# Kernel optimization log

Measured on AMD Instinct MI355X. Metric: run time of the kernel, lower is better.

Reference implementation:

```python
import jax, jax.numpy as jnp
import numpy as np

COST_CLASS, COST_MASK, COST_DICE = 1.0, 1.0, 1.0
ALPHA, GAMMA = 0.25, 2.0


def setup_inputs() -> dict:
    key = jax.random.key(0)
    k1, k2, k3, k4 = jax.random.split(key, 4)
    B, Q, C, H, W, T, Hm, Wm = 2, 100, 134, 256, 256, 20, 512, 512
    return {
        "masks_queries_logits": jax.random.normal(k1, (B, Q, H, W), jnp.float32),
        "class_queries_logits": jax.random.normal(k2, (B, Q, C), jnp.float32),
        "mask_labels": jax.random.uniform(k3, (B, T, Hm, Wm), dtype=jnp.float32),
        "class_labels": jax.random.randint(k4, (B, T), 0, C),
    }


def _nearest_resize(x, H, W):
    # torch F.interpolate(mode='nearest'): src_idx = floor(dst_idx * in / out)
    Hi, Wi = x.shape[-2], x.shape[-1]
    ri = (jnp.arange(H) * Hi) // H
    ci = (jnp.arange(W) * Wi) // W
    return x[..., ri, :][..., ci]


def _cost_matrices(masks_queries_logits, class_queries_logits, mask_labels, class_labels):
    B, Q, H, W = masks_queries_logits.shape
    HW = H * W
    tgt = _nearest_resize(mask_labels, H, W)                       # [B,T,H,W]
    probs = jax.nn.softmax(class_queries_logits, axis=-1)          # [B,Q,C]
    # cost_class = -probs[:, labels]  -> [B,Q,T]
    cost_class = -jnp.take_along_axis(
        probs, jnp.broadcast_to(class_labels[:, None, :], (B, Q, class_labels.shape[1])), axis=2
    )
    x = masks_queries_logits.reshape(B, Q, HW)                     # [B,Q,HW]
    lab = tgt.reshape(B, -1, HW)                                   # [B,T,HW]
    p = jax.nn.sigmoid(x)
    ce_pos = jax.nn.softplus(-x)   # BCEWithLogits(target=1)
    ce_neg = jax.nn.softplus(x)    # BCEWithLogits(target=0)
    focal_pos = ALPHA * (1.0 - p) ** GAMMA * ce_pos
    focal_neg = (1.0 - ALPHA) * p ** GAMMA * ce_neg
    cost_mask = (jnp.einsum('bqk,btk->bqt', focal_pos, lab)
                 + jnp.einsum('bqk,btk->bqt', focal_neg, 1.0 - lab)) / HW
    numer = 2.0 * jnp.einsum('bqk,btk->bqt', p, lab)
    denom = p.sum(-1)[:, :, None] + lab.sum(-1)[:, None, :]
    cost_dice = 1.0 - (numer + 1.0) / (denom + 1.0)
    return COST_MASK * cost_mask + COST_CLASS * cost_class + COST_DICE * cost_dice


def _hungarian(cost):
    # Exact O(n^3) Hungarian (Jonker-Volgenant style potentials), numpy on host.
    # Zero-pads to square like the torch code; dummy cols all-zero so the real
    # assignment equals the rectangular optimum.
    n_rows, n_cols = cost.shape
    n = max(n_rows, n_cols)
    a = np.zeros((n + 1, n + 1), dtype=np.float64)
    a[1:n_rows + 1, 1:n_cols + 1] = cost
    u = np.zeros(n + 1); v = np.zeros(n + 1)
    p = np.zeros(n + 1, dtype=np.int64)
    way = np.zeros(n + 1, dtype=np.int64)
    for i in range(1, n + 1):
        p[0] = i; j0 = 0
        minv = np.full(n + 1, np.inf)
        used = np.zeros(n + 1, dtype=bool)
        while True:
            used[j0] = True
            i0 = p[j0]
            cur = a[i0, 1:] - u[i0] - v[1:]
            free = ~used[1:]
            upd = free & (cur < minv[1:])
            minv[1:][upd] = cur[upd]
            way[1:][upd] = j0
            cand = np.where(free, minv[1:], np.inf)
            j1 = int(np.argmin(cand)) + 1
            delta = cand[j1 - 1]
            u[p[used]] += delta
            v[used] -= delta
            minv[1:][free] -= delta
            j0 = j1
            if p[j0] == 0:
                break
        while j0:
            j1 = way[j0]
            p[j0] = p[j1]
            j0 = j1
    rows, cols = [], []
    for j in range(1, n_cols + 1):
        r = p[j] - 1
        if 0 <= r < n_rows:
            rows.append(r); cols.append(j - 1)
    rows = np.asarray(rows, dtype=np.int64)
    cols = np.asarray(cols, dtype=np.int64)
    order = np.argsort(rows)  # torch impl emits pairs in ascending row order
    return rows[order], cols[order]


def reference(masks_queries_logits, class_queries_logits, mask_labels, class_labels):
    cost = _cost_matrices(masks_queries_logits, class_queries_logits, mask_labels, class_labels)
    cost_np = np.asarray(jax.device_get(cost), dtype=np.float64)  # [B,Q,T]
    pairs = [np.stack(_hungarian(c)) for c in cost_np]            # each [2, min(Q,T)]
    return jnp.asarray(np.stack(pairs), dtype=jnp.int32)          # [B, 2, T]
```

## Files before the change

### kernel.cpp

```cpp
#include <hip/hip_runtime.h>
#include <hip/hip_bf16.h>
#include <math.h>

#define HW_   65536
#define B_    2
#define Q_    100
#define C_    134
#define T_    20
#define NHUN  100
#define MT_   7
#define KSB   128
#define BKCH  512
#define WKCH  128
#define PREC  1088

typedef __attribute__((ext_vector_type(8))) short bf16x8;
typedef __attribute__((ext_vector_type(4))) float f32x4;

#define LABPS_OFF  0
#define CC_OFF     512
#define COST_OFF   4608
#define BASE_END   8704
#define LABT_HI_F  BASE_END
#define PART_OFF   (LABT_HI_F + 1310720)
#define CSUM_OFF   (PART_OFF + B_ * KSB * MT_ * PREC)
#define WS_END_F   (CSUM_OFF + B_ * MT_ * 1056)

__device__ inline unsigned short f2bf(float f) {
    unsigned int u = __builtin_bit_cast(unsigned int, f);
    u += 0x7FFFu + ((u >> 16) & 1u);
    return (unsigned short)(u >> 16);
}
__device__ inline float softplusf(float x) {
    float ax = fabsf(x);
    return fmaxf(x, 0.0f) + log1pf(expf(-ax));
}

__global__ void lab_prep_kernel(const float* __restrict__ ml, unsigned short* __restrict__ labT,
                                float* __restrict__ lab_ps, int writeT) {
    int b = blockIdx.x, t = blockIdx.y, ksl = blockIdx.z;
    int tid = threadIdx.x;
    const float* src = ml + (size_t)(b * T_ + t) * 262144;
    size_t dst = ((size_t)(b * T_ + t)) << 16;
    float acc = 0.f;
    for (int it = 0; it < 8; ++it) {
        int k = ksl * 8192 + it * 1024 + tid * 4;
        int r = k >> 8, c = k & 255;
        const float* s = src + r * 1024 + 2 * c;
        float4 u = *(const float4*)s;
        float4 w = *(const float4*)(s + 4);
        float v[4] = {u.x, u.z, w.x, w.z};
        unsigned short h[4];
#pragma unroll
        for (int e = 0; e < 4; ++e) { h[e] = f2bf(v[e]); acc += v[e]; }
        if (writeT) *(ushort4*)(labT + dst + k) = make_ushort4(h[0], h[1], h[2], h[3]);
    }
    for (int off = 32; off > 0; off >>= 1) acc += __shfl_down(acc, off);
    __shared__ float sb[4];
    int wid = tid >> 6, lane = tid & 63;
    if (lane == 0) sb[wid] = acc;
    __syncthreads();
    if (tid == 0) lab_ps[(b * T_ + t) * 8 + ksl] = sb[0] + sb[1] + sb[2] + sb[3];
}

__global__ void class_cost_kernel(const float* __restrict__ cl, const int* __restrict__ labels,
                                  float* __restrict__ cc) {
    int bq  = blockIdx.x;
    int b   = bq / Q_;
    int tid = threadIdx.x;
    __shared__ float sl[C_];
    const float* src = cl + (size_t)bq * C_;
    for (int c = tid; c < C_; c += 64) sl[c] = src[c];
    __syncthreads();
    float mx = -INFINITY;
    for (int c = tid; c < C_; c += 64) mx = fmaxf(mx, sl[c]);
    for (int off = 32; off > 0; off >>= 1) mx = fmaxf(mx, __shfl_xor(mx, off));
    float se = 0.f;
    for (int c = tid; c < C_; c += 64) se += expf(sl[c] - mx);
    for (int off = 32; off > 0; off >>= 1) se += __shfl_xor(se, off);
    float inv = 1.0f / se;
    if (tid < T_) {
        int lbl = labels[b * T_ + tid];
        cc[bq * T_ + tid] = -expf(sl[lbl] - mx) * inv;
    }
}

__global__ __launch_bounds__(256) void focal_mfma_kernel(
        const float* __restrict__ mq, const unsigned short* __restrict__ labT,
        float* __restrict__ part) {
    int idx = blockIdx.x;
    int mt  = idx % MT_;
    int rem = idx / MT_;
    int ks  = rem % KSB;
    int b   = rem / KSB;
    int tid  = threadIdx.x;
    int wave = tid >> 6, lane = tid & 63;
    int lg = lane >> 4, lr = lane & 15;

    int q = mt * 16 + lr;
    bool qok = (q < Q_);
    const float* xrow = mq + ((size_t)(b * Q_ + (qok ? q : 0)) << 16);
    int koff = ks * BKCH + wave * WKCH + lg * 8;

    const unsigned short* b1 = labT + (((size_t)(b * T_ + lr)) << 16);
    const unsigned short* b2 = labT + (((size_t)(b * T_ + 16 + (lr & 3))) << 16);
    bool n2row = (lr < 4);

    f32x4 accD0 = {0,0,0,0}, accD1 = {0,0,0,0};
    f32x4 accP0 = {0,0,0,0}, accP1 = {0,0,0,0};
    float F = 0.f, P = 0.f;

    bf16x8 zer;
#pragma unroll
    for (int e = 0; e < 8; ++e) zer[e] = 0;

    for (int kk = 0; kk < 4; ++kk) {
        int kb = koff + kk * 32;
        float4 u0 = *(const float4*)(xrow + kb);
        float4 u1 = *(const float4*)(xrow + kb + 4);
        float xv[8] = {u0.x, u0.y, u0.z, u0.w, u1.x, u1.y, u1.z, u1.w};

        bf16x8 f1 = *(const bf16x8*)(b1 + kb);
        bf16x8 f2 = n2row ? *(const bf16x8*)(b2 + kb) : zer;

        bf16x8 dh, ph;
#pragma unroll
        for (int e = 0; e < 8; ++e) {
            float x  = xv[e];
            float ax = fabsf(x);
            float a  = __expf(-ax);
            float rr = 1.0f / (1.0f + a);
            float p  = (x >= 0.f) ? rr : a * rr;
            float om = (x >= 0.f) ? a * rr : rr;
            float l1 = __logf(1.0f + a);
            float spn = fmaxf(-x, 0.f) + l1;
            float spp = spn + x;
            float fp = 0.25f * om * om * spn;
            float fn = 0.75f * p * p * spp;
            F += fn; P += p;
            dh[e] = (short)f2bf(fp - fn);
            ph[e] = (short)f2bf(p);
        }
        accD0 = __builtin_amdgcn_mfma_f32_16x16x32_bf16(dh, f1, accD0, 0, 0, 0);
        accD1 = __builtin_amdgcn_mfma_f32_16x16x32_bf16(dh, f2, accD1, 0, 0, 0);
        accP0 = __builtin_amdgcn_mfma_f32_16x16x32_bf16(ph, f1, accP0, 0, 0, 0);
        accP1 = __builtin_amdgcn_mfma_f32_16x16x32_bf16(ph, f2, accP1, 0, 0, 0);
    }

    F += __shfl_down(F, 32); F += __shfl_down(F, 16);
    P += __shfl_down(P, 32); P += __shfl_down(P, 16);

    __shared__ float red[4][4][64][4];
    __shared__ float fpb[4][2][16];
#pragma unroll
    for (int r = 0; r < 4; ++r) {
        red[wave][0][lane][r] = accD0[r];
        red[wave][1][lane][r] = accD1[r];
        red[wave][2][lane][r] = accP0[r];
        red[wave][3][lane][r] = accP1[r];
    }
    if (lane < 16) { fpb[wave][0][lane] = F; fpb[wave][1][lane] = P; }
    __syncthreads();
    for (int e = tid; e < 1024; e += 256) {
        int f  = e >> 8;
        int l2 = (e & 255) >> 2;
        int r  = e & 3;
        part[(size_t)idx * PREC + e] =
            red[0][f][l2][r] + red[1][f][l2][r] + red[2][f][l2][r] + red[3][f][l2][r];
    }
    if (tid < 16)
        part[(size_t)idx * PREC + 1024 + tid] =
            fpb[0][0][tid] + fpb[1][0][tid] + fpb[2][0][tid] + fpb[3][0][tid];
    else if (tid < 32) {
        int l = tid - 16;
        part[(size_t)idx * PREC + 1040 + l] =
            fpb[0][1][l] + fpb[1][1][l] + fpb[2][1][l] + fpb[3][1][l];
    }
}

__global__ __launch_bounds__(256) void reduce_part_kernel(const float* __restrict__ part,
                                                          float* __restrict__ Csum) {
    int bm   = blockIdx.x;
    int mt   = bm % MT_;
    int b    = bm / MT_;
    int tid  = threadIdx.x;
    int epos = tid & 31;
    int grp  = tid >> 5;
    int e    = blockIdx.y * 32 + epos;

    const float* base = part + (size_t)((b * KSB) * MT_ + mt) * PREC + e;
    float s = 0.f;
    for (int k = 0; k < 16; ++k) {
        s += base[(size_t)(grp * 16 + k) * MT_ * PREC];
    }
    __shared__ float red[8][33];
    red[grp][epos] = s;
    __syncthreads();
    if (tid < 32) {
        float tot = 0.f;
        for (int g = 0; g < 8; ++g) tot += red[g][tid];
        Csum[(size_t)bm * 1056 + e] = tot;
    }
}

__global__ __launch_bounds__(320) void compose_kernel(
        const float* __restrict__ Csum, const float* __restrict__ cl,
        const int* __restrict__ labels, const float* __restrict__ lab_ps,
        float* __restrict__ cost) {
    int bm = blockIdx.x;
    int mt = bm % MT_;
    int b  = bm / MT_;
    int tid = threadIdx.x;
    int q0 = mt * 16;

    __shared__ float sl[16][136];
    __shared__ float mx[16], se[16];
    __shared__ int   lbl[T_];
    for (int e = tid; e < 16 * C_; e += 320) {
        int qm = e / C_, c = e % C_;
        int q = q0 + qm;
        sl[qm][c] = (q < Q_) ? cl[(size_t)(b * Q_ + q) * C_ + c] : 0.f;
    }
    if (tid < T_) lbl[tid] = labels[b * T_ + tid];
    __syncthreads();
    if (tid < 16) {
        float m = -INFINITY;
        for (int c = 0; c < C_; ++c) m = fmaxf(m, sl[tid][c]);
        float s = 0.f;
        for (int c = 0; c < C_; ++c) s += expf(sl[tid][c] - m);
        mx[tid] = m; se[tid] = s;
    }
    __syncthreads();

    int qm = tid / T_, t = tid % T_;
    int q = q0 + qm;
    if (qm < 16 && q < Q_) {
        const float* C = Csum + (size_t)bm * 1056;
        int nt   = t >> 4;
        int lane = ((qm >> 2) << 4) | (t & 15);
        int reg  = qm & 3;
        float Sd = C[(0 + nt) * 256 + lane * 4 + reg];
        float Sp = C[(2 + nt) * 256 + lane * 4 + reg];
        float F  = C[1024 + qm];
        float P  = C[1040 + qm];
        float L = 0.f;
        for (int s8 = 0; s8 < 8; ++s8) L += lab_ps[(b * T_ + t) * 8 + s8];
        float ccv = -expf(sl[qm][lbl[t]] - mx[qm]) / se[qm];
        float cm = (Sd + F) * (1.0f / (float)HW_);
        float cd = 1.0f - (2.0f * Sp + 1.0f) / (P + L + 1.0f);
        cost[(size_t)(b * Q_ + q) * T_ + t] = cm + cd + ccv;
    }
}

__global__ __launch_bounds__(1024) void mask_cost_mono_kernel(
        const float* __restrict__ mq, const float* __restrict__ ml,
        const float* __restrict__ cc, const float* __restrict__ lab_ps,
        float* __restrict__ cost) {
    int bq  = blockIdx.x;
    int b   = bq / Q_;
    int tid = threadIdx.x;
    const float* xb  = mq + (size_t)bq * HW_;
    const float* mlb = ml + (size_t)b * T_ * 262144;
    float s1[T_], s2[T_];
#pragma unroll
    for (int t = 0; t < T_; ++t) { s1[t] = 0.f; s2[t] = 0.f; }
    float F = 0.f, P = 0.f;
    for (int k = tid; k < HW_; k += 1024) {
        int i = k >> 8, j = k & 255;
        float x = xb[k];
        float p = 1.0f / (1.0f + expf(-x));
        float spn = softplusf(-x);
        float spp = softplusf(x);
        float om = 1.0f - p;
        float fp = 0.25f * om * om * spn;
        float fn = 0.75f * p * p * spp;
        F += fn; P += p;
        float diff = fp - fn;
        int off0 = i * 1024 + 2 * j;
#pragma unroll
        for (int t = 0; t < T_; ++t) {
            float lab = mlb[t * 262144 + off0];
            s1[t] = fmaf(diff, lab, s1[t]);
            s2[t] = fmaf(p,    lab, s2[t]);
        }
    }
    __shared__ float sbuf[16][42];
    int wid = tid >> 6, lane = tid & 63;
#pragma unroll
    for (int t = 0; t < T_; ++t) {
        for (int off = 32; off > 0; off >>= 1) {
            s1[t] += __shfl_down(s1[t], off);
            s2[t] += __shfl_down(s2[t], off);
        }
    }
    for (int off = 32; off > 0; off >>= 1) { F += __shfl_down(F, off); P += __shfl_down(P, off); }
    if (lane == 0) {
#pragma unroll
        for (int t = 0; t < T_; ++t) { sbuf[wid][t] = s1[t]; sbuf[wid][T_ + t] = s2[t]; }
        sbuf[wid][40] = F; sbuf[wid][41] = P;
    }
    __syncthreads();
    if (tid < T_) {
        float S1 = 0.f, S2 = 0.f, Fs = 0.f, Ps = 0.f;
        for (int w = 0; w < 16; ++w) {
            S1 += sbuf[w][tid]; S2 += sbuf[w][T_ + tid];
            Fs += sbuf[w][40];  Ps += sbuf[w][41];
        }
        float L = 0.f;
        for (int sl = 0; sl < 8; ++sl) L += lab_ps[(b * T_ + tid) * 8 + sl];
        float cm = (S1 + Fs) * (1.0f / (float)HW_);
        float cd = 1.0f - (2.0f * S2 + 1.0f) / (Ps + L + 1.0f);
        cost[bq * T_ + tid] = cm + cd + cc[bq * T_ + tid];
    }
}

__global__ __launch_bounds__(64) void hungarian_kernel(const float* __restrict__ cost,
                                                       int* __restrict__ out) {
    int b    = blockIdx.x;
    int lane = threadIdx.x;

    __shared__ float csh[Q_ * T_];
    __shared__ float u[T_ + 1];
    __shared__ int   p[NHUN + 1];
    __shared__ int   way[NHUN + 1];

    for (int idx = lane; idx < Q_ * T_; idx += 64) csh[idx] = cost[b * Q_ * T_ + idx];
    for (int j = lane; j <= NHUN; j += 64) { p[j] = 0; way[j] = 0; }
    if (lane <= T_) u[lane] = 0.f;
    __syncthreads();

    const int ja = lane;
    const int jb = lane + 64;
    const bool jb_ok = (jb <= NHUN);
    float v_a = 0.f, v_b = 0.f;

    for (int i = 1; i <= T_; ++i) {
        if (lane == 0) p[0] = i;
        float m_a = INFINITY, m_b = INFINITY;
        bool us_a = false, us_b = false;
        __syncthreads();
        int j0 = 0;
        while (true) {
            if (ja == j0) us_a = true;
            if (jb == j0) us_b = true;
            int   i0  = p[j0];
            float ui0 = u[i0];
            bool fa = (!us_a && ja >= 1);
            bool fb = (jb_ok && !us_b);
            if (fa) {
                float cur = csh[(ja - 1) * T_ + (i0 - 1)] - ui0 - v_a;
                if (cur < m_a) { m_a = cur; way[ja] = j0; }
            }
            if (fb) {
                float cur = csh[(jb - 1) * T_ + (i0 - 1)] - ui0 - v_b;
                if (cur < m_b) { m_b = cur; way[jb] = j0; }
            }
            float ca = fa ? m_a : INFINITY;
            float cb = fb ? m_b : INFINITY;
            float vmin = fminf(ca, cb);
            for (int off = 32; off > 0; off >>= 1)
                vmin = fminf(vmin, __shfl_xor(vmin, off));
            unsigned long long ba = __ballot(ca == vmin);
            int j1;
            if (ba) j1 = __ffsll(ba) - 1;
            else    j1 = __ffsll(__ballot(cb == vmin)) - 1 + 64;
            float delta = vmin;
            if (us_a) { u[p[ja]] += delta; v_a -= delta; } else { m_a -= delta; }
            if (jb_ok) {
                if (us_b) { u[p[jb]] += delta; v_b -= delta; } else { m_b -= delta; }
            }
            __threadfence_block();
            j0 = j1;
            if (p[j0] == 0) break;
        }
        if (lane == 0) {
            int jj = j0;
            while (jj) { int jn = way[jj]; p[jj] = p[jn]; jj = jn; }
        }
        __syncthreads();
    }

    if (lane == 0) {
        int* ob = out + b * 2 * T_;
        int k = 0;
        for (int j = 1; j <= NHUN; ++j) {
            if (p[j] != 0) { ob[k] = j - 1; ob[T_ + k] = p[j] - 1; ++k; }
        }
    }
}

extern "C" void kernel_launch(void* const* d_in, const int* in_sizes, int n_in,
                              void* d_out, int out_size, void* d_ws, size_t ws_size,
                              hipStream_t stream) {
    const float* mq     = (const float*)d_in[0];
    const float* cl     = (const float*)d_in[1];
    const float* ml     = (const float*)d_in[2];
    const int*   labels = (const int*)d_in[3];
    int* out = (int*)d_out;
    float* ws = (float*)d_ws;

    float* lab_ps = ws + LABPS_OFF;
    float* cc     = ws + CC_OFF;
    float* cost   = ws + COST_OFF;

    size_t need = (size_t)WS_END_F * 4;

    if (ws_size >= need) {
        unsigned short* labT = (unsigned short*)(ws + LABT_HI_F);
        float* part = ws + PART_OFF;
        float* Csum = ws + CSUM_OFF;
        hipLaunchKernelGGL(lab_prep_kernel,   dim3(B_, T_, 8), dim3(256), 0, stream,
                           ml, labT, lab_ps, 1);
        hipLaunchKernelGGL(focal_mfma_kernel, dim3(B_ * KSB * MT_), dim3(256), 0, stream,
                           mq, labT, part);
        hipLaunchKernelGGL(reduce_part_kernel, dim3(B_ * MT_, 33), dim3(256), 0, stream,
                           part, Csum);
        hipLaunchKernelGGL(compose_kernel,    dim3(B_ * MT_),  dim3(320), 0, stream,
                           Csum, cl, labels, lab_ps, cost);
    } else {
        hipLaunchKernelGGL(lab_prep_kernel,   dim3(B_, T_, 8), dim3(256), 0, stream,
                           ml, (unsigned short*)ws, lab_ps, 0);
        hipLaunchKernelGGL(class_cost_kernel, dim3(B_ * Q_),   dim3(64),  0, stream, cl, labels, cc);
        hipLaunchKernelGGL(mask_cost_mono_kernel, dim3(B_ * Q_), dim3(1024), 0, stream,
                           mq, ml, cc, lab_ps, cost);
    }
    hipLaunchKernelGGL(hungarian_kernel, dim3(B_), dim3(64), 0, stream, cost, out);
}
```

Measured before the change: 77.01 us.

## Pre-swizzle label fragments and stage focal operands through LDS for MFMA

Label masks are now written in an MFMA-fragment-ordered bf16 layout, split into two buffers with the T=16..19 block zero-padded, so each lane does one contiguous 16-byte load per chunk. The focal kernel now reads query logits as coalesced float4 rows across threads, computes the focal and sigmoid terms, and stores them to a swizzled LDS tile. Waves then read A fragments from LDS for the MFMAs. This removes strided per-lane global loads and branches, at the cost of an extra barrier, 33KB of LDS per block, and more shuffle reductions for the F/P sums.

After: 84.98 us. 1.1x slower.

```diff
diff --git a/kernel.cpp b/kernel.cpp
--- a/kernel.cpp
+++ b/kernel.cpp
@@ -11,8 +11,8 @@
 #define MT_   7
 #define KSB   128
 #define BKCH  512
-#define WKCH  128
 #define PREC  1088
+#define NCH   2048
 
 typedef __attribute__((ext_vector_type(8))) short bf16x8;
 typedef __attribute__((ext_vector_type(4))) float f32x4;
@@ -21,10 +21,11 @@
 #define CC_OFF     512
 #define COST_OFF   4608
 #define BASE_END   8704
-#define LABT_HI_F  BASE_END
-#define PART_OFF   (LABT_HI_F + 1310720)
-#define CSUM_OFF   (PART_OFF + B_ * KSB * MT_ * PREC)
-#define WS_END_F   (CSUM_OFF + B_ * MT_ * 1056)
+#define LABF1_F   BASE_END
+#define LABF2_F   (LABF1_F + 1048576)
+#define PART_OFF  (LABF2_F + 1048576)
+#define CSUM_OFF  (PART_OFF + B_ * KSB * MT_ * PREC)
+#define WS_END_F  (CSUM_OFF + B_ * MT_ * 1056)
 
 __device__ inline unsigned short f2bf(float f) {
     unsigned int u = __builtin_bit_cast(unsigned int, f);
@@ -36,12 +37,12 @@
     return fmaxf(x, 0.0f) + log1pf(expf(-ax));
 }
 
-__global__ void lab_prep_kernel(const float* __restrict__ ml, unsigned short* __restrict__ labT,
-                                float* __restrict__ lab_ps, int writeT) {
+__global__ void lab_prep_kernel(const float* __restrict__ ml, unsigned short* __restrict__ labF1,
+                                unsigned short* __restrict__ labF2, float* __restrict__ lab_ps,
+                                int writeT) {
     int b = blockIdx.x, t = blockIdx.y, ksl = blockIdx.z;
     int tid = threadIdx.x;
     const float* src = ml + (size_t)(b * T_ + t) * 262144;
-    size_t dst = ((size_t)(b * T_ + t)) << 16;
     float acc = 0.f;
     for (int it = 0; it < 8; ++it) {
         int k = ksl * 8192 + it * 1024 + tid * 4;
@@ -53,7 +54,24 @@
         unsigned short h[4];
 #pragma unroll
         for (int e = 0; e < 4; ++e) { h[e] = f2bf(v[e]); acc += v[e]; }
-        if (writeT) *(ushort4*)(labT + dst + k) = make_ushort4(h[0], h[1], h[2], h[3]);
+        if (writeT) {
+            int ch = k >> 5;
+            int g  = (k >> 3) & 3;
+            int e0 = k & 7;
+            uint2 val;
+            val.x = (unsigned)h[0] | ((unsigned)h[1] << 16);
+            val.y = (unsigned)h[2] | ((unsigned)h[3] << 16);
+            if (t < 16) {
+                *(uint2*)(labF1 + ((size_t)(b * NCH + ch) * 64 + t + 16 * g) * 8 + e0) = val;
+            } else {
+                int lr = t - 16;
+                *(uint2*)(labF2 + ((size_t)(b * NCH + ch) * 64 + lr + 16 * g) * 8 + e0) = val;
+                uint2 z = {0u, 0u};
+#pragma unroll
+                for (int m = 1; m <= 3; ++m)
+                    *(uint2*)(labF2 + ((size_t)(b * NCH + ch) * 64 + (lr + 4 * m) + 16 * g) * 8 + e0) = z;
+            }
+        }
     }
     for (int off = 32; off > 0; off >>= 1) acc += __shfl_down(acc, off);
     __shared__ float sb[4];
@@ -86,8 +104,8 @@
 }
 
 __global__ __launch_bounds__(256) void focal_mfma_kernel(
-        const float* __restrict__ mq, const unsigned short* __restrict__ labT,
-        float* __restrict__ part) {
+        const float* __restrict__ mq, const unsigned short* __restrict__ labF1,
+        const unsigned short* __restrict__ labF2, float* __restrict__ part) {
     int idx = blockIdx.x;
     int mt  = idx % MT_;
     int rem = idx / MT_;
@@ -95,63 +113,73 @@
     int b   = rem / KSB;
     int tid  = threadIdx.x;
     int wave = tid >> 6, lane = tid & 63;
-    int lg = lane >> 4, lr = lane & 15;
-
-    int q = mt * 16 + lr;
-    bool qok = (q < Q_);
-    const float* xrow = mq + ((size_t)(b * Q_ + (qok ? q : 0)) << 16);
-    int koff = ks * BKCH + wave * WKCH + lg * 8;
-
-    const unsigned short* b1 = labT + (((size_t)(b * T_ + lr)) << 16);
-    const unsigned short* b2 = labT + (((size_t)(b * T_ + 16 + (lr & 3))) << 16);
-    bool n2row = (lr < 4);
-
-    f32x4 accD0 = {0,0,0,0}, accD1 = {0,0,0,0};
-    f32x4 accP0 = {0,0,0,0}, accP1 = {0,0,0,0};
-    float F = 0.f, P = 0.f;
-
-    bf16x8 zer;
-#pragma unroll
-    for (int e = 0; e < 8; ++e) zer[e] = 0;
-
-    for (int kk = 0; kk < 4; ++kk) {
-        int kb = koff + kk * 32;
-        float4 u0 = *(const float4*)(xrow + kb);
-        float4 u1 = *(const float4*)(xrow + kb + 4);
-        float xv[8] = {u0.x, u0.y, u0.z, u0.w, u1.x, u1.y, u1.z, u1.w};
-
-        bf16x8 f1 = *(const bf16x8*)(b1 + kb);
-        bf16x8 f2 = n2row ? *(const bf16x8*)(b2 + kb) : zer;
-
-        bf16x8 dh, ph;
-#pragma unroll
-        for (int e = 0; e < 8; ++e) {
-            float x  = xv[e];
+    int lr = lane & 15, lg = lane >> 4;
+
+    __shared__ char smem[33344];
+
+    int grp = tid >> 7;
+    int kk4 = (tid & 127) * 4;
+    float Fa[8], Pa[8];
+#pragma unroll
+    for (int p = 0; p < 8; ++p) {
+        int r = p * 2 + grp;
+        int q = mt * 16 + r;
+        const float* xr = mq + ((size_t)(b * Q_ + (q < Q_ ? q : 0)) << 16) + ks * BKCH + kk4;
+        float4 xv = *(const float4*)xr;
+        unsigned short dh[4], ph[4];
+        float Fs = 0.f, Ps = 0.f;
+#pragma unroll
+        for (int e = 0; e < 4; ++e) {
+            float x  = (&xv.x)[e];
             float ax = fabsf(x);
             float a  = __expf(-ax);
             float rr = 1.0f / (1.0f + a);
-            float p  = (x >= 0.f) ? rr : a * rr;
+            float p_ = (x >= 0.f) ? rr : a * rr;
             float om = (x >= 0.f) ? a * rr : rr;
             float l1 = __logf(1.0f + a);
             float spn = fmaxf(-x, 0.f) + l1;
             float spp = spn + x;
             float fp = 0.25f * om * om * spn;
-            float fn = 0.75f * p * p * spp;
-            F += fn; P += p;
-            dh[e] = (short)f2bf(fp - fn);
-            ph[e] = (short)f2bf(p);
-        }
-        accD0 = __builtin_amdgcn_mfma_f32_16x16x32_bf16(dh, f1, accD0, 0, 0, 0);
-        accD1 = __builtin_amdgcn_mfma_f32_16x16x32_bf16(dh, f2, accD1, 0, 0, 0);
-        accP0 = __builtin_amdgcn_mfma_f32_16x16x32_bf16(ph, f1, accP0, 0, 0, 0);
-        accP1 = __builtin_amdgcn_mfma_f32_16x16x32_bf16(ph, f2, accP1, 0, 0, 0);
-    }
-
-    F += __shfl_down(F, 32); F += __shfl_down(F, 16);
-    P += __shfl_down(P, 32); P += __shfl_down(P, 16);
-
-    __shared__ float red[4][4][64][4];
-    __shared__ float fpb[4][2][16];
+            float fn = 0.75f * p_ * p_ * spp;
+            Fs += fn; Ps += p_;
+            dh[e] = f2bf(fp - fn);
+            ph[e] = f2bf(p_);
+        }
+        Fa[p] = Fs; Pa[p] = Ps;
+        int wr = r * 1024 + ((((kk4 >> 3)) ^ (r & 7)) << 4) + ((kk4 & 4) << 1);
+        uint2 dv, pv;
+        dv.x = (unsigned)dh[0] | ((unsigned)dh[1] << 16);
+        dv.y = (unsigned)dh[2] | ((unsigned)dh[3] << 16);
+        pv.x = (unsigned)ph[0] | ((unsigned)ph[1] << 16);
+        pv.y = (unsigned)ph[2] | ((unsigned)ph[3] << 16);
+        *(uint2*)(smem + wr)         = dv;
+        *(uint2*)(smem + 16384 + wr) = pv;
+    }
+    __syncthreads();
+
+    f32x4 accD0 = {0,0,0,0}, accD1 = {0,0,0,0};
+    f32x4 accP0 = {0,0,0,0}, accP1 = {0,0,0,0};
+#pragma unroll
+    for (int kk = 0; kk < 4; ++kk) {
+        int blk = wave * 16 + kk * 4 + lg;
+        int ad  = lr * 1024 + ((blk ^ (lr & 7)) << 4);
+        bf16x8 adh = *(const bf16x8*)(smem + ad);
+        bf16x8 aph = *(const bf16x8*)(smem + 16384 + ad);
+        int c = ks * (BKCH / 32) + wave * 4 + kk;
+        const unsigned short* f1p = labF1 + ((size_t)(b * NCH + c) * 64 + lane) * 8;
+        const unsigned short* f2p = labF2 + ((size_t)(b * NCH + c) * 64 + lane) * 8;
+        bf16x8 f1 = *(const bf16x8*)f1p;
+        bf16x8 f2 = *(const bf16x8*)f2p;
+        accD0 = __builtin_amdgcn_mfma_f32_16x16x32_bf16(adh, f1, accD0, 0, 0, 0);
+        accD1 = __builtin_amdgcn_mfma_f32_16x16x32_bf16(adh, f2, accD1, 0, 0, 0);
+        accP0 = __builtin_amdgcn_mfma_f32_16x16x32_bf16(aph, f1, accP0, 0, 0, 0);
+        accP1 = __builtin_amdgcn_mfma_f32_16x16x32_bf16(aph, f2, accP1, 0, 0, 0);
+    }
+    __syncthreads();
+
+    float (*red)[4][64][4] = (float (*)[4][64][4])smem;
+    float (*wfpF)[8] = (float (*)[8])(smem + 16384);
+    float (*wfpP)[8] = (float (*)[8])(smem + 16384 + 128);
 #pragma unroll
     for (int r = 0; r < 4; ++r) {
         red[wave][0][lane][r] = accD0[r];
@@ -159,7 +187,15 @@
         red[wave][2][lane][r] = accP0[r];
         red[wave][3][lane][r] = accP1[r];
     }
-    if (lane < 16) { fpb[wave][0][lane] = F; fpb[wave][1][lane] = P; }
+#pragma unroll
+    for (int p = 0; p < 8; ++p) {
+        float f = Fa[p], pp = Pa[p];
+        for (int off = 32; off > 0; off >>= 1) {
+            f  += __shfl_down(f, off);
+            pp += __shfl_down(pp, off);
+        }
+        if (lane == 0) { wfpF[wave][p] = f; wfpP[wave][p] = pp; }
+    }
     __syncthreads();
     for (int e = tid; e < 1024; e += 256) {
         int f  = e >> 8;
@@ -168,13 +204,10 @@
         part[(size_t)idx * PREC + e] =
             red[0][f][l2][r] + red[1][f][l2][r] + red[2][f][l2][r] + red[3][f][l2][r];
     }
-    if (tid < 16)
-        part[(size_t)idx * PREC + 1024 + tid] =
-            fpb[0][0][tid] + fpb[1][0][tid] + fpb[2][0][tid] + fpb[3][0][tid];
-    else if (tid < 32) {
-        int l = tid - 16;
-        part[(size_t)idx * PREC + 1040 + l] =
-            fpb[0][1][l] + fpb[1][1][l] + fpb[2][1][l] + fpb[3][1][l];
+    if (tid < 16) {
+        int p = tid >> 1, g = tid & 1;
+        part[(size_t)idx * PREC + 1024 + tid] = wfpF[2 * g][p] + wfpF[2 * g + 1][p];
+        part[(size_t)idx * PREC + 1040 + tid] = wfpP[2 * g][p] + wfpP[2 * g + 1][p];
     }
 }
 
@@ -406,20 +439,21 @@
     size_t need = (size_t)WS_END_F * 4;
 
     if (ws_size >= need) {
-        unsigned short* labT = (unsigned short*)(ws + LABT_HI_F);
+        unsigned short* labF1 = (unsigned short*)(ws + LABF1_F);
+        unsigned short* labF2 = (unsigned short*)(ws + LABF2_F);
         float* part = ws + PART_OFF;
         float* Csum = ws + CSUM_OFF;
         hipLaunchKernelGGL(lab_prep_kernel,   dim3(B_, T_, 8), dim3(256), 0, stream,
-                           ml, labT, lab_ps, 1);
+                           ml, labF1, labF2, lab_ps, 1);
         hipLaunchKernelGGL(focal_mfma_kernel, dim3(B_ * KSB * MT_), dim3(256), 0, stream,
-                           mq, labT, part);
+                           mq, labF1, labF2, part);
         hipLaunchKernelGGL(reduce_part_kernel, dim3(B_ * MT_, 33), dim3(256), 0, stream,
                            part, Csum);
         hipLaunchKernelGGL(compose_kernel,    dim3(B_ * MT_),  dim3(320), 0, stream,
                            Csum, cl, labels, lab_ps, cost);
     } else {
         hipLaunchKernelGGL(lab_prep_kernel,   dim3(B_, T_, 8), dim3(256), 0, stream,
-                           ml, (unsigned short*)ws, lab_ps, 0);
+                           ml, (unsigned short*)ws, (unsigned short*)ws, lab_ps, 0);
         hipLaunchKernelGGL(class_cost_kernel, dim3(B_ * Q_),   dim3(64),  0, stream, cl, labels, cc);
         hipLaunchKernelGGL(mask_cost_mono_kernel, dim3(B_ * Q_), dim3(1024), 0, stream,
                            mq, ml, cc, lab_ps, cost);
```

## Pre-swizzle bf16 label masks into MFMA fragment layout for coalesced loads

Applied to the files above, without the earlier changes.

The label prep kernel now stages all 20 target rows for a k-slice in shared memory and writes them out pre-arranged in the per-lane MFMA B-fragment order, with a second zero-padded buffer for targets 16-19. The focal MFMA kernel then reads each fragment as one contiguous 16-byte-per-lane load instead of strided per-target rows, and the conditional zero fill goes away. Label partial sums are split over 64 slices instead of 8, and the prep grid changes shape accordingly. This trades a heavier prep kernel and a padded second buffer for better-coalesced operand traffic in the main kernel.

New measurement: 86.16 us. 11.9% more time.

```diff
diff --git a/kernel.cpp b/kernel.cpp
--- a/kernel.cpp
+++ b/kernel.cpp
@@ -11,20 +11,23 @@
 #define MT_   7
 #define KSB   128
 #define BKCH  512
-#define WKCH  128
 #define PREC  1088
+#define NCH   2048
+#define NSL   64
+#define LPSL  1040
 
 typedef __attribute__((ext_vector_type(8))) short bf16x8;
 typedef __attribute__((ext_vector_type(4))) float f32x4;
 
 #define LABPS_OFF  0
-#define CC_OFF     512
-#define COST_OFF   4608
-#define BASE_END   8704
-#define LABT_HI_F  BASE_END
-#define PART_OFF   (LABT_HI_F + 1310720)
-#define CSUM_OFF   (PART_OFF + B_ * KSB * MT_ * PREC)
-#define WS_END_F   (CSUM_OFF + B_ * MT_ * 1056)
+#define CC_OFF     2560
+#define COST_OFF   6560
+#define BASE_END   10560
+#define LABF1_F   BASE_END
+#define LABF2_F   (LABF1_F + 1048576)
+#define PART_OFF  (LABF2_F + 1048576)
+#define CSUM_OFF  (PART_OFF + B_ * KSB * MT_ * PREC)
+#define WS_END_F  (CSUM_OFF + B_ * MT_ * 1056)
 
 __device__ inline unsigned short f2bf(float f) {
     unsigned int u = __builtin_bit_cast(unsigned int, f);
@@ -36,31 +39,62 @@
     return fmaxf(x, 0.0f) + log1pf(expf(-ax));
 }
 
-__global__ void lab_prep_kernel(const float* __restrict__ ml, unsigned short* __restrict__ labT,
-                                float* __restrict__ lab_ps, int writeT) {
-    int b = blockIdx.x, t = blockIdx.y, ksl = blockIdx.z;
+__global__ __launch_bounds__(256) void lab_prep_kernel(
+        const float* __restrict__ ml, unsigned short* __restrict__ labF1,
+        unsigned short* __restrict__ labF2, float* __restrict__ lab_ps, int writeT) {
+    int b   = blockIdx.x;
+    int sl  = blockIdx.y;
     int tid = threadIdx.x;
-    const float* src = ml + (size_t)(b * T_ + t) * 262144;
-    size_t dst = ((size_t)(b * T_ + t)) << 16;
-    float acc = 0.f;
-    for (int it = 0; it < 8; ++it) {
-        int k = ksl * 8192 + it * 1024 + tid * 4;
-        int r = k >> 8, c = k & 255;
-        const float* s = src + r * 1024 + 2 * c;
+    int kb  = sl * 1024;
+
+    __shared__ unsigned short tile[T_ * LPSL];
+    __shared__ float rb[4][T_];
+
+    float acc[T_];
+    int k0 = kb + tid * 4;
+    int r  = k0 >> 8, c = k0 & 255;
+    int goff = r * 1024 + 2 * c;
+#pragma unroll
+    for (int t = 0; t < T_; ++t) {
+        const float* s = ml + (size_t)(b * T_ + t) * 262144 + goff;
         float4 u = *(const float4*)s;
         float4 w = *(const float4*)(s + 4);
         float v[4] = {u.x, u.z, w.x, w.z};
-        unsigned short h[4];
-#pragma unroll
-        for (int e = 0; e < 4; ++e) { h[e] = f2bf(v[e]); acc += v[e]; }
-        if (writeT) *(ushort4*)(labT + dst + k) = make_ushort4(h[0], h[1], h[2], h[3]);
-    }
-    for (int off = 32; off > 0; off >>= 1) acc += __shfl_down(acc, off);
-    __shared__ float sb[4];
-    int wid = tid >> 6, lane = tid & 63;
-    if (lane == 0) sb[wid] = acc;
-    __syncthreads();
-    if (tid == 0) lab_ps[(b * T_ + t) * 8 + ksl] = sb[0] + sb[1] + sb[2] + sb[3];
+        acc[t] = v[0] + v[1] + v[2] + v[3];
+        unsigned short h0 = f2bf(v[0]), h1 = f2bf(v[1]), h2 = f2bf(v[2]), h3 = f2bf(v[3]);
+        uint2 pk;
+        pk.x = (unsigned)h0 | ((unsigned)h1 << 16);
+        pk.y = (unsigned)h2 | ((unsigned)h3 << 16);
+        *(uint2*)(tile + t * LPSL + tid * 4) = pk;
+    }
+    __syncthreads();
+
+    if (writeT) {
+        unsigned short* o1 = labF1 + (size_t)(b * NCH + sl * 32) * 512;
+        unsigned short* o2 = labF2 + (size_t)(b * NCH + sl * 32) * 512;
+        for (int w = tid; w < 2048; w += 256) {
+            int lane = w & 63;
+            int chl  = w >> 6;
+            int ts = lane & 15, g = lane >> 4;
+            int kl = chl * 32 + g * 8;
+            uint4 v1 = *(const uint4*)(tile + ts * LPSL + kl);
+            *(uint4*)(o1 + (size_t)w * 8) = v1;
+            uint4 v2 = {0u, 0u, 0u, 0u};
+            if (ts < 4) v2 = *(const uint4*)(tile + (16 + ts) * LPSL + kl);
+            *(uint4*)(o2 + (size_t)w * 8) = v2;
+        }
+    }
+
+    int wid = tid >> 6, lane_ = tid & 63;
+#pragma unroll
+    for (int t = 0; t < T_; ++t) {
+        float a = acc[t];
+        for (int off = 32; off > 0; off >>= 1) a += __shfl_down(a, off);
+        if (lane_ == 0) rb[wid][t] = a;
+    }
+    __syncthreads();
+    if (tid < T_)
+        lab_ps[(b * T_ + tid) * NSL + sl] = rb[0][tid] + rb[1][tid] + rb[2][tid] + rb[3][tid];
 }
 
 __global__ void class_cost_kernel(const float* __restrict__ cl, const int* __restrict__ labels,
@@ -86,8 +120,8 @@
 }
 
 __global__ __launch_bounds__(256) void focal_mfma_kernel(
-        const float* __restrict__ mq, const unsigned short* __restrict__ labT,
-        float* __restrict__ part) {
+        const float* __restrict__ mq, const unsigned short* __restrict__ labF1,
+        const unsigned short* __restrict__ labF2, float* __restrict__ part) {
     int idx = blockIdx.x;
     int mt  = idx % MT_;
     int rem = idx / MT_;
@@ -100,19 +134,14 @@
     int q = mt * 16 + lr;
     bool qok = (q < Q_);
     const float* xrow = mq + ((size_t)(b * Q_ + (qok ? q : 0)) << 16);
-    int koff = ks * BKCH + wave * WKCH + lg * 8;
-
-    const unsigned short* b1 = labT + (((size_t)(b * T_ + lr)) << 16);
-    const unsigned short* b2 = labT + (((size_t)(b * T_ + 16 + (lr & 3))) << 16);
-    bool n2row = (lr < 4);
+    int koff = ks * BKCH + wave * 128 + lg * 8;
+
+    const unsigned short* f1base = labF1 + (size_t)(b * NCH) * 512 + lane * 8;
+    const unsigned short* f2base = labF2 + (size_t)(b * NCH) * 512 + lane * 8;
 
     f32x4 accD0 = {0,0,0,0}, accD1 = {0,0,0,0};
     f32x4 accP0 = {0,0,0,0}, accP1 = {0,0,0,0};
     float F = 0.f, P = 0.f;
-
-    bf16x8 zer;
-#pragma unroll
-    for (int e = 0; e < 8; ++e) zer[e] = 0;
 
     for (int kk = 0; kk < 4; ++kk) {
         int kb = koff + kk * 32;
@@ -120,8 +149,9 @@
         float4 u1 = *(const float4*)(xrow + kb + 4);
         float xv[8] = {u0.x, u0.y, u0.z, u0.w, u1.x, u1.y, u1.z, u1.w};
 
-        bf16x8 f1 = *(const bf16x8*)(b1 + kb);
-        bf16x8 f2 = n2row ? *(const bf16x8*)(b2 + kb) : zer;
+        int c = ks * 16 + wave * 4 + kk;
+        bf16x8 f1 = *(const bf16x8*)(f1base + (size_t)c * 512);
+        bf16x8 f2 = *(const bf16x8*)(f2base + (size_t)c * 512);
 
         bf16x8 dh, ph;
 #pragma unroll
@@ -244,7 +274,7 @@
         float F  = C[1024 + qm];
         float P  = C[1040 + qm];
         float L = 0.f;
-        for (int s8 = 0; s8 < 8; ++s8) L += lab_ps[(b * T_ + t) * 8 + s8];
+        for (int s8 = 0; s8 < NSL; ++s8) L += lab_ps[(b * T_ + t) * NSL + s8];
         float ccv = -expf(sl[qm][lbl[t]] - mx[qm]) / se[qm];
         float cm = (Sd + F) * (1.0f / (float)HW_);
         float cd = 1.0f - (2.0f * Sp + 1.0f) / (P + L + 1.0f);
@@ -307,7 +337,7 @@
             Fs += sbuf[w][40];  Ps += sbuf[w][41];
         }
         float L = 0.f;
-        for (int sl = 0; sl < 8; ++sl) L += lab_ps[(b * T_ + tid) * 8 + sl];
+        for (int sl = 0; sl < NSL; ++sl) L += lab_ps[(b * T_ + tid) * NSL + sl];
         float cm = (S1 + Fs) * (1.0f / (float)HW_);
         float cd = 1.0f - (2.0f * S2 + 1.0f) / (Ps + L + 1.0f);
         cost[bq * T_ + tid] = cm + cd + cc[bq * T_ + tid];
@@ -406,20 +436,21 @@
     size_t need = (size_t)WS_END_F * 4;
 
     if (ws_size >= need) {
-        unsigned short* labT = (unsigned short*)(ws + LABT_HI_F);
+        unsigned short* labF1 = (unsigned short*)(ws + LABF1_F);
+        unsigned short* labF2 = (unsigned short*)(ws + LABF2_F);
         float* part = ws + PART_OFF;
         float* Csum = ws + CSUM_OFF;
-        hipLaunchKernelGGL(lab_prep_kernel,   dim3(B_, T_, 8), dim3(256), 0, stream,
-                           ml, labT, lab_ps, 1);
+        hipLaunchKernelGGL(lab_prep_kernel,   dim3(B_, NSL),  dim3(256), 0, stream,
+                           ml, labF1, labF2, lab_ps, 1);
         hipLaunchKernelGGL(focal_mfma_kernel, dim3(B_ * KSB * MT_), dim3(256), 0, stream,
-                           mq, labT, part);
+                           mq, labF1, labF2, part);
         hipLaunchKernelGGL(reduce_part_kernel, dim3(B_ * MT_, 33), dim3(256), 0, stream,
                            part, Csum);
         hipLaunchKernelGGL(compose_kernel,    dim3(B_ * MT_),  dim3(320), 0, stream,
                            Csum, cl, labels, lab_ps, cost);
     } else {
-        hipLaunchKernelGGL(lab_prep_kernel,   dim3(B_, T_, 8), dim3(256), 0, stream,
-                           ml, (unsigned short*)ws, lab_ps, 0);
+        hipLaunchKernelGGL(lab_prep_kernel,   dim3(B_, NSL),  dim3(256), 0, stream,
+                           ml, (unsigned short*)ws, (unsigned short*)ws, lab_ps, 0);
         hipLaunchKernelGGL(class_cost_kernel, dim3(B_ * Q_),   dim3(64),  0, stream, cl, labels, cc);
         hipLaunchKernelGGL(mask_cost_mono_kernel, dim3(B_ * Q_), dim3(1024), 0, stream,
                            mq, ml, cc, lab_ps, cost);
```

## Keep Hungarian state in registers with wave shuffles and add greedy initial assignment

Applied to the files above, without the earlier changes.

The single-wavefront Hungarian kernel now holds the potentials u, v, the row assignment p and the back-pointers way in per-lane registers. Values move between lanes with shuffles and ballots instead of LDS arrays, fences and block barriers. A greedy pass first sets each target row's potential to its row minimum and assigns that column when it is free. Only rows still unassigned then go through the full augmenting-path loop. The cost tile in LDS is padded to a stride of 21 to reduce bank conflicts, at the price of more shuffles per step and a tie-breaking order that may differ from the reference.

Result: faster. 70.89 us (-8.0%).

```diff
diff --git a/kernel.cpp b/kernel.cpp
--- a/kernel.cpp
+++ b/kernel.cpp
@@ -11,8 +11,8 @@
 #define MT_   7
 #define KSB   128
 #define BKCH  512
-#define WKCH  128
 #define PREC  1088
+#define CPAD  21
 
 typedef __attribute__((ext_vector_type(8))) short bf16x8;
 typedef __attribute__((ext_vector_type(4))) float f32x4;
@@ -100,7 +100,7 @@
     int q = mt * 16 + lr;
     bool qok = (q < Q_);
     const float* xrow = mq + ((size_t)(b * Q_ + (qok ? q : 0)) << 16);
-    int koff = ks * BKCH + wave * WKCH + lg * 8;
+    int koff = ks * BKCH + wave * 128 + lg * 8;
 
     const unsigned short* b1 = labT + (((size_t)(b * T_ + lr)) << 16);
     const unsigned short* b2 = labT + (((size_t)(b * T_ + 16 + (lr & 3))) << 16);
@@ -319,41 +319,66 @@
     int b    = blockIdx.x;
     int lane = threadIdx.x;
 
-    __shared__ float csh[Q_ * T_];
-    __shared__ float u[T_ + 1];
-    __shared__ int   p[NHUN + 1];
-    __shared__ int   way[NHUN + 1];
-
-    for (int idx = lane; idx < Q_ * T_; idx += 64) csh[idx] = cost[b * Q_ * T_ + idx];
-    for (int j = lane; j <= NHUN; j += 64) { p[j] = 0; way[j] = 0; }
-    if (lane <= T_) u[lane] = 0.f;
+    __shared__ float csh[Q_ * CPAD];
+    __shared__ int   psh[NHUN + 1];
+
+    for (int j = lane; j < Q_; j += 64) {
+#pragma unroll
+        for (int t = 0; t < T_; ++t)
+            csh[j * CPAD + t] = cost[b * Q_ * T_ + j * T_ + t];
+    }
     __syncthreads();
 
     const int ja = lane;
     const int jb = lane + 64;
+    const bool ja_ok = (ja >= 1);
     const bool jb_ok = (jb <= NHUN);
+
+    int   p_a = 0, p_b = 0;
     float v_a = 0.f, v_b = 0.f;
+    float u_reg = 0.f;
 
     for (int i = 1; i <= T_; ++i) {
-        if (lane == 0) p[0] = i;
+        float ca = ja_ok ? csh[(ja - 1) * CPAD + (i - 1)] : INFINITY;
+        float cb = jb_ok ? csh[(jb - 1) * CPAD + (i - 1)] : INFINITY;
+        float vmin = fminf(ca, cb);
+        for (int off = 32; off > 0; off >>= 1)
+            vmin = fminf(vmin, __shfl_xor(vmin, off));
+        unsigned long long ba = __ballot(ca == vmin);
+        int j1 = ba ? (__ffsll(ba) - 1) : (__ffsll(__ballot(cb == vmin)) - 1 + 64);
+        if (lane == i) u_reg = vmin;
+        int pj = __shfl((j1 < 64) ? p_a : p_b, j1 & 63);
+        if (pj == 0) {
+            if (j1 < 64) { if (lane == j1) p_a = i; }
+            else         { if (lane == j1 - 64) p_b = i; }
+        }
+    }
+
+    for (int i = 1; i <= T_; ++i) {
+        bool mine = (p_a == i) || (p_b == i);
+        if (__ballot(mine)) continue;
+
         float m_a = INFINITY, m_b = INFINITY;
-        bool us_a = false, us_b = false;
-        __syncthreads();
-        int j0 = 0;
+        int   way_a = 0, way_b = 0;
+        bool  us_a = false, us_b = false;
+        bool  in_tree = (lane == i);
+        int   j0 = 0, jf;
+
         while (true) {
+            int i0 = (j0 == 0) ? i : __shfl((j0 < 64) ? p_a : p_b, j0 & 63);
+            if (lane == i0) in_tree = true;
+            float ui0 = __shfl(u_reg, i0);
             if (ja == j0) us_a = true;
             if (jb == j0) us_b = true;
-            int   i0  = p[j0];
-            float ui0 = u[i0];
-            bool fa = (!us_a && ja >= 1);
-            bool fb = (jb_ok && !us_b);
+            bool fa = ja_ok && !us_a;
+            bool fb = jb_ok && !us_b;
             if (fa) {
-                float cur = csh[(ja - 1) * T_ + (i0 - 1)] - ui0 - v_a;
-                if (cur < m_a) { m_a = cur; way[ja] = j0; }
+                float cur = csh[(ja - 1) * CPAD + (i0 - 1)] - ui0 - v_a;
+                if (cur < m_a) { m_a = cur; way_a = j0; }
             }
             if (fb) {
-                float cur = csh[(jb - 1) * T_ + (i0 - 1)] - ui0 - v_b;
-                if (cur < m_b) { m_b = cur; way[jb] = j0; }
+                float cur = csh[(jb - 1) * CPAD + (i0 - 1)] - ui0 - v_b;
+                if (cur < m_b) { m_b = cur; way_b = j0; }
             }
             float ca = fa ? m_a : INFINITY;
             float cb = fb ? m_b : INFINITY;
@@ -361,30 +386,34 @@
             for (int off = 32; off > 0; off >>= 1)
                 vmin = fminf(vmin, __shfl_xor(vmin, off));
             unsigned long long ba = __ballot(ca == vmin);
-            int j1;
-            if (ba) j1 = __ffsll(ba) - 1;
-            else    j1 = __ffsll(__ballot(cb == vmin)) - 1 + 64;
+            int j1 = ba ? (__ffsll(ba) - 1) : (__ffsll(__ballot(cb == vmin)) - 1 + 64);
             float delta = vmin;
-            if (us_a) { u[p[ja]] += delta; v_a -= delta; } else { m_a -= delta; }
-            if (jb_ok) {
-                if (us_b) { u[p[jb]] += delta; v_b -= delta; } else { m_b -= delta; }
-            }
-            __threadfence_block();
+            if (us_a) v_a -= delta; else m_a -= delta;
+            if (us_b) v_b -= delta; else m_b -= delta;
+            if (in_tree) u_reg += delta;
             j0 = j1;
-            if (p[j0] == 0) break;
-        }
-        if (lane == 0) {
-            int jj = j0;
-            while (jj) { int jn = way[jj]; p[jj] = p[jn]; jj = jn; }
-        }
-        __syncthreads();
-    }
-
+            int pj0 = __shfl((j0 < 64) ? p_a : p_b, j0 & 63);
+            if (pj0 == 0) { jf = j0; break; }
+        }
+        int jj = jf;
+        while (jj) {
+            int wv = __shfl((jj < 64) ? way_a : way_b, jj & 63);
+            int pn = (wv == 0) ? i : __shfl((wv < 64) ? p_a : p_b, wv & 63);
+            if (jj < 64) { if (lane == jj) p_a = pn; }
+            else         { if (lane == jj - 64) p_b = pn; }
+            jj = wv;
+        }
+    }
+
+    if (ja_ok) psh[ja] = p_a;
+    if (jb_ok) psh[jb] = p_b;
+    if (lane == 0) psh[0] = 0;
+    __syncthreads();
     if (lane == 0) {
         int* ob = out + b * 2 * T_;
         int k = 0;
         for (int j = 1; j <= NHUN; ++j) {
-            if (p[j] != 0) { ob[k] = j - 1; ob[T_ + k] = p[j] - 1; ++k; }
+            if (psh[j] != 0) { ob[k] = j - 1; ob[T_ + k] = psh[j] - 1; ++k; }
         }
     }
 }
```
